# Optimization experiments

Measured on AMD Instinct MI355X. Metric: run time of the kernel, lower is better.

The kernel has to match this reference:

```python
import jax, jax.numpy as jnp
import numpy as np
import math

B, N, T, D, H, NOUT = 32, 20, 100, 4, 128, 16
E = N * (N - 1)
EPS = 1e-5

def _conv1d(x, w, b):
    # x: [M, Cin, L], w: [Cout, Cin, K] -> [M, Cout, L-K+1] (VALID, stride 1)
    y = jax.lax.conv_general_dilated(x, w, (1,), 'VALID', dimension_numbers=('NCH', 'OIH', 'NCH'))
    return y + b[None, :, None]

def _bn(x, g, b, axes, caxis):
    # training-mode batch norm (biased variance), eps as in torch
    m = jnp.mean(x, axis=axes, keepdims=True)
    v = jnp.var(x, axis=axes, keepdims=True)
    sh = [1] * x.ndim
    sh[caxis] = -1
    return (x - m) / jnp.sqrt(v + EPS) * g.reshape(sh) + b.reshape(sh)

def _mlp(x, w1, b1, w2, b2, g, bb):
    h = jax.nn.elu(x @ w1.T + b1)
    h = jax.nn.elu(h @ w2.T + b2)
    return _bn(h, g, bb, (0, 1), 2)  # BN over B*E samples per feature

def _forward(rel_rec, rel_send, inputs, conv1_w, conv1_b, bn1_g, bn1_b, conv2_w, conv2_b, bn2_g, bn2_b, pred_w, pred_b, att_w, att_b, mlp1_w1, mlp1_b1, mlp1_w2, mlp1_b2, mlp1_g, mlp1_bb, mlp2_w1, mlp2_b1, mlp2_w2, mlp2_b2, mlp2_g, mlp2_bb, mlp3_w1, mlp3_b1, mlp3_w2, mlp3_b2, mlp3_g, mlp3_bb, fc_out_w, fc_out_b):
    Bv, Nv, Tv, Dv = inputs.shape
    Ev = Nv * (Nv - 1)
    # node2edge_temporal: gather sender/receiver trajectories -> [B*E, 2D, T]
    xf = inputs.reshape(Bv, Nv, Tv * Dv)
    recv = jnp.einsum('en,bnf->bef', rel_rec, xf).reshape(Bv * Ev, Tv, Dv).transpose(0, 2, 1)
    send = jnp.einsum('en,bnf->bef', rel_send, xf).reshape(Bv * Ev, Tv, Dv).transpose(0, 2, 1)
    edges = jnp.concatenate([send, recv], axis=1)
    # CNN over time
    h = jax.nn.relu(_conv1d(edges, conv1_w, conv1_b))
    h = _bn(h, bn1_g, bn1_b, (0, 2), 1)
    L = h.shape[-1] // 2
    h = h[:, :, : 2 * L].reshape(h.shape[0], h.shape[1], L, 2).max(axis=-1)  # maxpool k=2 s=2
    h = jax.nn.relu(_conv1d(h, conv2_w, conv2_b))
    h = _bn(h, bn2_g, bn2_b, (0, 2), 1)
    pred = jnp.einsum('bct,oc->bot', h, pred_w[:, :, 0]) + pred_b[None, :, None]
    att = jax.nn.softmax(jnp.einsum('bct,oc->bot', h, att_w[:, :, 0]) + att_b[None, :, None], axis=-1)
    x = (pred * att).mean(axis=-1).reshape(Bv, Ev, -1)  # attention-weighted mean pool
    x = _mlp(x, mlp1_w1, mlp1_b1, mlp1_w2, mlp1_b2, mlp1_g, mlp1_bb)
    x_skip = x
    # edge2node: scatter-mean into receivers (divide by N)
    xn = jnp.einsum('en,beh->bnh', rel_rec, x) / Nv
    xn = _mlp(xn, mlp2_w1, mlp2_b1, mlp2_w2, mlp2_b2, mlp2_g, mlp2_bb)
    # node2edge: gather back to edges
    es = jnp.einsum('en,bnh->beh', rel_send, xn)
    er = jnp.einsum('en,bnh->beh', rel_rec, xn)
    x = jnp.concatenate([es, er, x_skip], axis=2)
    x = _mlp(x, mlp3_w1, mlp3_b1, mlp3_w2, mlp3_b2, mlp3_g, mlp3_bb)
    return x @ fc_out_w.T + fc_out_b

def setup_inputs() -> dict:
    key = jax.random.key(0)
    ks = iter(jax.random.split(key, 64))
    def rn(shape, scale):
        return jax.random.normal(next(ks), shape, dtype=jnp.float32) * scale
    def xav(fo, fi):
        return rn((fo, fi), math.sqrt(2.0 / (fo + fi)))
    inputs = rn((B, N, T, D), 1.0)
    pairs = np.array([(i, j) for i in range(N) for j in range(N) if i != j])
    eye = np.eye(N, dtype=np.float32)
    d = {'inputs': inputs,
         'rel_rec': jnp.asarray(eye[pairs[:, 0]]),
         'rel_send': jnp.asarray(eye[pairs[:, 1]])}
    d['conv1_w'] = rn((H, 2 * D, 5), math.sqrt(2.0 / (5 * H)))
    d['conv1_b'] = jnp.full((H,), 0.1, jnp.float32)
    d['bn1_g'] = jnp.ones((H,), jnp.float32); d['bn1_b'] = jnp.zeros((H,), jnp.float32)
    d['conv2_w'] = rn((H, H, 5), math.sqrt(2.0 / (5 * H)))
    d['conv2_b'] = jnp.full((H,), 0.1, jnp.float32)
    d['bn2_g'] = jnp.ones((H,), jnp.float32); d['bn2_b'] = jnp.zeros((H,), jnp.float32)
    d['pred_w'] = rn((H, H, 1), math.sqrt(2.0 / H))
    d['pred_b'] = jnp.full((H,), 0.1, jnp.float32)
    d['att_w'] = rn((1, H, 1), math.sqrt(2.0))
    d['att_b'] = jnp.full((1,), 0.1, jnp.float32)
    for nm, fi in (('mlp1', H), ('mlp2', H), ('mlp3', 3 * H)):
        d[nm + '_w1'] = xav(H, fi); d[nm + '_b1'] = jnp.full((H,), 0.1, jnp.float32)
        d[nm + '_w2'] = xav(H, H); d[nm + '_b2'] = jnp.full((H,), 0.1, jnp.float32)
        d[nm + '_g'] = jnp.ones((H,), jnp.float32); d[nm + '_bb'] = jnp.zeros((H,), jnp.float32)
    d['fc_out_w'] = xav(NOUT, H)
    d['fc_out_b'] = jnp.full((NOUT,), 0.1, jnp.float32)
    return d

def reference(inputs, rel_rec, rel_send, conv1_w, conv1_b, bn1_g, bn1_b, conv2_w, conv2_b, bn2_g, bn2_b, pred_w, pred_b, att_w, att_b, mlp1_w1, mlp1_b1, mlp1_w2, mlp1_b2, mlp1_g, mlp1_bb, mlp2_w1, mlp2_b1, mlp2_w2, mlp2_b2, mlp2_g, mlp2_bb, mlp3_w1, mlp3_b1, mlp3_w2, mlp3_b2, mlp3_g, mlp3_bb, fc_out_w, fc_out_b):
    return _forward(rel_rec, rel_send, inputs, conv1_w, conv1_b, bn1_g, bn1_b, conv2_w, conv2_b, bn2_g, bn2_b, pred_w, pred_b, att_w, att_b, mlp1_w1, mlp1_b1, mlp1_w2, mlp1_b2, mlp1_g, mlp1_bb, mlp2_w1, mlp2_b1, mlp2_w2, mlp2_b2, mlp2_g, mlp2_bb, mlp3_w1, mlp3_b1, mlp3_w2, mlp3_b2, mlp3_g, mlp3_bb, fc_out_w, fc_out_b)
```

## Files before the change

kernel.cpp:

```cpp
#include <hip/hip_runtime.h>
#include <hip/hip_bf16.h>
#include <hip/hip_fp16.h>

#define BB 32
#define NN 20
#define TT 100
#define DD 4
#define HH 128
#define EE 380
#define BE 12160
#define L1 96
#define LP 48
#define L2 44
#define NOUT 16
#define EPS 1e-5f
#define NREP 64

typedef _Float16 f16x8 __attribute__((ext_vector_type(8)));
typedef _Float16 f16x4 __attribute__((ext_vector_type(4)));
typedef _Float16 f16x2 __attribute__((ext_vector_type(2)));
typedef float f32x4 __attribute__((ext_vector_type(4)));

#define S_BN1_SC 256
#define S_BN2_SC 768
#define S_M1_SC 1280
#define S_M2_SC 1792
#define S_M3_SC 2304

#define OFF_STATS 0ULL
#define OFF_SIDX 16384ULL
#define OFF_RIDX 18432ULL
#define OFF_INC 20480ULL
#define OFF_Y23 24576ULL
#define OFF_X 149446656ULL
#define OFF_BUFA 155672576ULL
#define OFF_BUFB 161898496ULL
#define OFF_XN 168124416ULL
#define OFF_T640 168452096ULL
#define OFF_REPM 168779776ULL
#define OFF_HF16 168845312ULL
#define OFF_MP 171958272ULL
#define OFF_APACK OFF_T640
#define OFF_APACK1 (OFF_T640 + 163840ULL)
#define OFF_PWT (OFF_T640 + 180224ULL)
#define OFF_REP1 OFF_BUFA
#define OFF_REP2 (OFF_BUFA + 65536ULL)
#define MP_M1W1 0
#define MP_M1W2 16384
#define MP_M2W1 32768
#define MP_M2W2 49152
#define MP_M3W2 65536
#define MP_M3W1 81920

__device__ __forceinline__ float eluf(float v) { return v > 0.f ? v : expm1f(v); }

__global__ __launch_bounds__(256) void k_prep(const float* __restrict__ rel_rec,
                                              const float* __restrict__ rel_send,
                                              const float* __restrict__ w2,
                                              const float* __restrict__ w1,
                                              const float* __restrict__ pred_w,
                                              const float* __restrict__ m1w1,
                                              const float* __restrict__ m1w2,
                                              const float* __restrict__ m2w1,
                                              const float* __restrict__ m2w2,
                                              const float* __restrict__ m3w1,
                                              const float* __restrict__ m3w2,
                                              _Float16* __restrict__ apack,
                                              _Float16* __restrict__ apack1,
                                              float* __restrict__ pwt,
                                              _Float16* __restrict__ mp,
                                              float* rep1, float* rep2, float* repm,
                                              int* sidx, int* ridx, int* inc) {
    int b = blockIdx.x;
    int tid = threadIdx.x;
    int l = tid & 63;
    if (b < 40) {
        int f = b * 4 + (tid >> 6);
        int m0 = f & 7, ks = f >> 3, s = ks & 3, k = ks >> 2;
        int m = m0 * 16 + (l & 15);
        int cbase = 32 * s + (l >> 4) * 8;
#pragma unroll
        for (int j = 0; j < 8; ++j)
            apack[(f * 64 + l) * 8 + j] = (_Float16)w2[m * 640 + (cbase + j) * 5 + k];
    } else if (b < 44) {
        int f = (b - 40) * 4 + (tid >> 6);
        int m0 = f & 7, s = f >> 3;
        int m = m0 * 16 + (l & 15);
        int cbase = 32 * s + (l >> 4) * 8;
#pragma unroll
        for (int j = 0; j < 8; ++j) {
            int c = cbase + j;
            int k = c >> 3, ci = c & 7;
            apack1[(f * 64 + l) * 8 + j] = (k < 5) ? (_Float16)w1[m * 40 + ci * 5 + k]
                                                   : (_Float16)0.f;
        }
    } else if (b == 44) {
        for (int i = tid; i < NREP * 256; i += 256) { rep1[i] = 0.f; rep2[i] = 0.f; repm[i] = 0.f; }
        for (int e = tid; e < EE; e += 256) {
            int s = 0, r = 0;
            for (int n = 0; n < NN; ++n) {
                if (rel_send[e * NN + n] > 0.5f) s = n;
                if (rel_rec[e * NN + n] > 0.5f) r = n;
            }
            sidx[e] = s; ridx[e] = r;
        }
        __syncthreads();
        if (tid < NN) {
            int k = 0;
            for (int e = 0; e < EE; ++e)
                if (ridx[e] == tid) inc[tid * (NN - 1) + (k++)] = e;
        }
    } else if (b < 53) {
        int idx = (b - 45) * 2048 + tid;
        for (int rep = 0; rep < 8; ++rep, idx += 256) {
            int o = idx >> 7, c = idx & 127;
            pwt[c * 128 + o] = pred_w[idx];
        }
    } else {
        int idx = b - 53;
        const float* W; _Float16* dst; int K;
        if (idx < 8)       { W = m1w1; dst = mp + MP_M1W1; K = 128; }
        else if (idx < 16) { W = m1w2; dst = mp + MP_M1W2; K = 128; idx -= 8; }
        else if (idx < 24) { W = m2w1; dst = mp + MP_M2W1; K = 128; idx -= 16; }
        else if (idx < 32) { W = m2w2; dst = mp + MP_M2W2; K = 128; idx -= 24; }
        else if (idx < 40) { W = m3w2; dst = mp + MP_M3W2; K = 128; idx -= 32; }
        else               { W = m3w1; dst = mp + MP_M3W1; K = 384; idx -= 40; }
        int f = idx * 4 + (tid >> 6);
        int s = f >> 3, m0 = f & 7;
        int m = m0 * 16 + (l & 15);
        int cb = 32 * s + (l >> 4) * 8;
#pragma unroll
        for (int j = 0; j < 8; ++j)
            dst[(f * 64 + l) * 8 + j] = (_Float16)W[m * K + cb + j];
    }
}

__global__ __launch_bounds__(256) void k_conv1_stats(const float* __restrict__ inputs,
                                                     const _Float16* __restrict__ apack1,
                                                     const float* __restrict__ conv1_b,
                                                     const int* __restrict__ sidx,
                                                     const int* __restrict__ ridx,
                                                     float* rep1,
                                                     _Float16* __restrict__ y2p) {
    __shared__ __align__(16) _Float16 s_edgesT[104 * 8];
    __shared__ __align__(16) _Float16 s_y2t[48 * 136];
    int be = blockIdx.x;
    int b = be / EE, e = be - b * EE;
    int sn = sidx[e], rn = ridx[e];
    float* rep = rep1 + (be & (NREP - 1)) * 256;
    for (int i = threadIdx.x; i < 200; i += 256) {
        int side = (i >= 100) ? 1 : 0;
        int t = i - side * 100;
        int n = side ? rn : sn;
        float4 v = *(const float4*)(inputs + ((long long)(b * NN + n) * TT + t) * DD);
        f16x4 o = {(_Float16)v.x, (_Float16)v.y, (_Float16)v.z, (_Float16)v.w};
        *(f16x4*)(&s_edgesT[t * 8 + side * 4]) = o;
    }
    if (threadIdx.x < 32) s_edgesT[800 + threadIdx.x] = (_Float16)0.f;
    __syncthreads();
    int w = threadIdx.x >> 6, lane = threadIdx.x & 63;
    int quad = lane >> 4, l15 = lane & 15;
    f32x4 acc1[2][6];
#pragma unroll
    for (int m = 0; m < 2; ++m)
#pragma unroll
        for (int nt = 0; nt < 6; ++nt) acc1[m][nt] = (f32x4){0.f, 0.f, 0.f, 0.f};
    {
        const f16x8* Ap = (const f16x8*)apack1;
#pragma unroll
        for (int s = 0; s < 2; ++s) {
            f16x8 a0 = Ap[(s * 8 + 2 * w) * 64 + lane];
            f16x8 a1 = Ap[(s * 8 + 2 * w + 1) * 64 + lane];
#pragma unroll
            for (int nt = 0; nt < 6; ++nt) {
                f16x8 bfr = *(const f16x8*)(&s_edgesT[(nt * 16 + l15 + 4 * s + quad) * 8]);
                acc1[0][nt] = __builtin_amdgcn_mfma_f32_16x16x32_f16(a0, bfr, acc1[0][nt], 0, 0, 0);
                acc1[1][nt] = __builtin_amdgcn_mfma_f32_16x16x32_f16(a1, bfr, acc1[1][nt], 0, 0, 0);
            }
        }
    }
#pragma unroll
    for (int m = 0; m < 2; ++m) {
        int co0 = (2 * w + m) * 16 + quad * 4;
        float ss[4] = {0.f, 0.f, 0.f, 0.f}, qq[4] = {0.f, 0.f, 0.f, 0.f};
#pragma unroll
        for (int nt = 0; nt < 6; ++nt) {
            int t = nt * 16 + l15;
#pragma unroll
            for (int r = 0; r < 4; ++r) {
                float v = fmaxf(acc1[m][nt][r] + conv1_b[co0 + r], 0.f);
                ss[r] += v; qq[r] += v * v;
                float p = __shfl_xor(v, 1);
                if ((l15 & 1) == 0)
                    s_y2t[(t >> 1) * 136 + co0 + r] = (_Float16)fmaxf(v, p);
            }
        }
#pragma unroll
        for (int r = 0; r < 4; ++r) {
            float s = ss[r], q = qq[r];
            s += __shfl_xor(s, 1); s += __shfl_xor(s, 2); s += __shfl_xor(s, 4); s += __shfl_xor(s, 8);
            q += __shfl_xor(q, 1); q += __shfl_xor(q, 2); q += __shfl_xor(q, 4); q += __shfl_xor(q, 8);
            if (l15 == 0) {
                atomicAdd(&rep[co0 + r], s);
                atomicAdd(&rep[128 + co0 + r], q);
            }
        }
    }
    __syncthreads();
    _Float16* dst = y2p + (long long)be * 6144;
    for (int chunk = threadIdx.x; chunk < 768; chunk += 256) {
        int row = chunk >> 4, off = (chunk & 15) * 8;
        *(f16x8*)(dst + row * 128 + off) = *(const f16x8*)(&s_y2t[row * 136 + off]);
    }
}

__global__ void k_finalize_rep(float* __restrict__ rep, float* stats, int scIdx,
                               const float* __restrict__ g, const float* __restrict__ bb,
                               float inv_count) {
    int j = threadIdx.x;
    float s = 0.f, q = 0.f;
    for (int i = 0; i < NREP; ++i) {
        s += rep[i * 256 + j];
        q += rep[i * 256 + 128 + j];
    }
    for (int i = 0; i < NREP; ++i) {
        rep[i * 256 + j] = 0.f;
        rep[i * 256 + 128 + j] = 0.f;
    }
    float m = s * inv_count;
    float v = fmaxf(q * inv_count - m * m, 0.f);
    float sc = g[j] * rsqrtf(v + EPS);
    stats[scIdx + j] = sc;
    stats[scIdx + 128 + j] = bb[j] - m * sc;
}

__global__ __launch_bounds__(256) void k_conv2(_Float16* __restrict__ y23,
                                               const _Float16* __restrict__ apack,
                                               const float* __restrict__ conv2_b,
                                               const float* __restrict__ stats,
                                               float* rep2) {
    __shared__ __align__(16) _Float16 s_y2t[2][52 * 136];
    int tid = threadIdx.x;
    int be0 = blockIdx.x * 2;
    for (int i = tid; i < 544; i += 256) {
        int ed = i / 272, rem = i - ed * 272;
        ((int*)(&s_y2t[ed][48 * 136]))[rem] = 0;
    }
    {
        int c0 = (tid & 15) * 8;
        float4 sca = *(const float4*)(stats + S_BN1_SC + c0);
        float4 scb = *(const float4*)(stats + S_BN1_SC + c0 + 4);
        float4 sha = *(const float4*)(stats + S_BN1_SC + 128 + c0);
        float4 shb = *(const float4*)(stats + S_BN1_SC + 128 + c0 + 4);
        for (int i = tid; i < 1536; i += 256) {
            int ed = i / 768, rem = i - ed * 768;
            int row = rem >> 4;
            f16x8 g = *(const f16x8*)(y23 + (long long)(be0 + ed) * 6144 + row * 128 + c0);
            f16x8 o;
            o[0] = (_Float16)fmaf((float)g[0], sca.x, sha.x);
            o[1] = (_Float16)fmaf((float)g[1], sca.y, sha.y);
            o[2] = (_Float16)fmaf((float)g[2], sca.z, sha.z);
            o[3] = (_Float16)fmaf((float)g[3], sca.w, sha.w);
            o[4] = (_Float16)fmaf((float)g[4], scb.x, shb.x);
            o[5] = (_Float16)fmaf((float)g[5], scb.y, shb.y);
            o[6] = (_Float16)fmaf((float)g[6], scb.z, shb.z);
            o[7] = (_Float16)fmaf((float)g[7], scb.w, shb.w);
            *(f16x8*)(&s_y2t[ed][row * 136 + c0]) = o;
        }
    }
    __syncthreads();
    int w = tid >> 6, lane = tid & 63;
    int quad = lane >> 4, l15 = lane & 15;
    int g = w & 1, e = w >> 1;
    f32x4 acc[4][3];
#pragma unroll
    for (int m = 0; m < 4; ++m)
#pragma unroll
        for (int nt = 0; nt < 3; ++nt) acc[m][nt] = (f32x4){0.f, 0.f, 0.f, 0.f};
    const f16x8* Ap = (const f16x8*)apack;
    const char* base = (const char*)&s_y2t[e][0];
#pragma unroll
    for (int k = 0; k < 5; ++k) {
#pragma unroll
        for (int s = 0; s < 4; ++s) {
            f16x8 am[4];
#pragma unroll
            for (int m = 0; m < 4; ++m)
                am[m] = Ap[((k * 4 + s) * 8 + g * 4 + m) * 64 + lane];
#pragma unroll
            for (int nt = 0; nt < 3; ++nt) {
                f16x8 bfr = *(const f16x8*)(base + (nt * 16 + l15 + k) * 272 + 64 * s + quad * 16);
#pragma unroll
                for (int m = 0; m < 4; ++m)
                    acc[m][nt] = __builtin_amdgcn_mfma_f32_16x16x32_f16(am[m], bfr, acc[m][nt], 0, 0, 0);
            }
        }
    }
    int be = be0 + e;
    _Float16* y3 = y23 + (long long)be * 6144;
    float* rep = rep2 + (be & (NREP - 1)) * 256;
#pragma unroll
    for (int m = 0; m < 4; ++m) {
        int co0 = (g * 4 + m) * 16 + quad * 4;
        float ssum[4] = {0.f, 0.f, 0.f, 0.f}, qsum[4] = {0.f, 0.f, 0.f, 0.f};
#pragma unroll
        for (int nt = 0; nt < 3; ++nt) {
            int t = nt * 16 + l15;
            bool valid = t < 44;
#pragma unroll
            for (int r = 0; r < 4; ++r) {
                float v = fmaxf(acc[m][nt][r] + conv2_b[co0 + r], 0.f);
                if (valid) {
                    y3[(co0 + r) * 44 + t] = (_Float16)v;
                    ssum[r] += v; qsum[r] += v * v;
                }
            }
        }
#pragma unroll
        for (int r = 0; r < 4; ++r) {
            float s = ssum[r], q = qsum[r];
            s += __shfl_xor(s, 1); s += __shfl_xor(s, 2); s += __shfl_xor(s, 4); s += __shfl_xor(s, 8);
            q += __shfl_xor(q, 1); q += __shfl_xor(q, 2); q += __shfl_xor(q, 4); q += __shfl_xor(q, 8);
            if (l15 == 0) {
                atomicAdd(&rep[co0 + r], s);
                atomicAdd(&rep[128 + co0 + r], q);
            }
        }
    }
}

__global__ __launch_bounds__(256) void k_predatt(const _Float16* __restrict__ y23,
                                                 const float* __restrict__ stats,
                                                 const float* __restrict__ att_w,
                                                 const float* __restrict__ att_b,
                                                 const float* __restrict__ pwt,
                                                 const float* __restrict__ pred_b,
                                                 float* __restrict__ x) {
    __shared__ float h[128 * 45];
    __shared__ float s_att[48];
    __shared__ float s_p1[256];
    __shared__ float s_p2[256];
    __shared__ float s_sc[128], s_sh[128];
    int be = blockIdx.x, tid = threadIdx.x;
    if (tid < 128) {
        s_sc[tid] = stats[S_BN2_SC + tid];
        s_sh[tid] = stats[S_BN2_SC + 128 + tid];
    }
    __syncthreads();
    const f16x2* yp = (const f16x2*)(y23 + (long long)be * 6144);
    for (int i = tid; i < 2816; i += 256) {
        int c = i / 22, t2 = i - c * 22;
        f16x2 v = yp[i];
        float sc = s_sc[c], sh = s_sh[c];
        h[c * 45 + 2 * t2] = fmaf((float)v[0], sc, sh);
        h[c * 45 + 2 * t2 + 1] = fmaf((float)v[1], sc, sh);
    }
    __syncthreads();
    int w = tid >> 6, lane = tid & 63;
    {
        float aw0 = att_w[lane], aw1 = att_w[64 + lane];
        for (int tt = 0; tt < 11; ++tt) {
            int t = w * 11 + tt;
            float p = h[lane * 45 + t] * aw0 + h[(64 + lane) * 45 + t] * aw1;
            p += __shfl_xor(p, 1); p += __shfl_xor(p, 2); p += __shfl_xor(p, 4);
            p += __shfl_xor(p, 8); p += __shfl_xor(p, 16); p += __shfl_xor(p, 32);
            if (lane == 0) s_att[t] = p + att_b[0];
        }
    }
    __syncthreads();
    if (w == 0) {
        float v = (lane < 44) ? s_att[lane] : -1e30f;
        float m = v;
        m = fmaxf(m, __shfl_xor(m, 1)); m = fmaxf(m, __shfl_xor(m, 2));
        m = fmaxf(m, __shfl_xor(m, 4)); m = fmaxf(m, __shfl_xor(m, 8));
        m = fmaxf(m, __shfl_xor(m, 16)); m = fmaxf(m, __shfl_xor(m, 32));
        float ev = (lane < 44) ? expf(v - m) : 0.f;
        float ss = ev;
        ss += __shfl_xor(ss, 1); ss += __shfl_xor(ss, 2); ss += __shfl_xor(ss, 4);
        ss += __shfl_xor(ss, 8); ss += __shfl_xor(ss, 16); ss += __shfl_xor(ss, 32);
        if (lane < 44) s_att[lane] = ev / ss;
    }
    __syncthreads();
    {
        int c = tid & 127, hh = tid >> 7;
        float a = 0.f;
        for (int t = hh * 22; t < hh * 22 + 22; ++t) a = fmaf(h[c * 45 + t], s_att[t], a);
        s_p1[tid] = a;
    }
    __syncthreads();
    {
        int o = tid & 127, hh = tid >> 7;
        float a = 0.f;
        for (int c = hh * 64; c < hh * 64 + 64; ++c) {
            float hw = s_p1[c] + s_p1[128 + c];
            a = fmaf(pwt[c * 128 + o], hw, a);
        }
        s_p2[tid] = a;
    }
    __syncthreads();
    if (tid < 128) {
        float a = s_p2[tid] + s_p2[128 + tid] + pred_b[tid];
        x[(long long)be * 128 + tid] = a * (1.0f / 44.0f);
    }
}

template <bool IN16, bool OUT16, bool STATS>
__global__ __launch_bounds__(256) void k_linmm(const void* __restrict__ inV,
                                               const _Float16* __restrict__ wp,
                                               const float* __restrict__ bias,
                                               void* __restrict__ outV,
                                               float* __restrict__ repm) {
    __shared__ __align__(16) _Float16 s_b[64 * 136];
    int tid = threadIdx.x;
    long long r0 = (long long)blockIdx.x * 64;
    if (IN16) {
        const f16x8* src = (const f16x8*)((const _Float16*)inV + r0 * 128);
        for (int i = tid; i < 1024; i += 256) {
            int row = i >> 4, c0 = (i & 15) * 8;
            *(f16x8*)(&s_b[row * 136 + c0]) = src[i];
        }
    } else {
        const float4* src = (const float4*)((const float*)inV + r0 * 128);
        for (int i = tid; i < 2048; i += 256) {
            int row = i >> 5, c0 = (i & 31) * 4;
            float4 v = src[i];
            f16x4 o = {(_Float16)v.x, (_Float16)v.y, (_Float16)v.z, (_Float16)v.w};
            *(f16x4*)(&s_b[row * 136 + c0]) = o;
        }
    }
    __syncthreads();
    int w = tid >> 6, lane = tid & 63, quad = lane >> 4, l15 = lane & 15;
    f32x4 acc[2][4];
#pragma unroll
    for (int m = 0; m < 2; ++m)
#pragma unroll
        for (int nt = 0; nt < 4; ++nt) acc[m][nt] = (f32x4){0.f, 0.f, 0.f, 0.f};
    const f16x8* Ap = (const f16x8*)wp;
#pragma unroll
    for (int s = 0; s < 4; ++s) {
        f16x8 a0 = Ap[(s * 8 + 2 * w) * 64 + lane];
        f16x8 a1 = Ap[(s * 8 + 2 * w + 1) * 64 + lane];
#pragma unroll
        for (int nt = 0; nt < 4; ++nt) {
            f16x8 bfr = *(const f16x8*)((const char*)s_b + (nt * 16 + l15) * 272 + 64 * s + quad * 16);
            acc[0][nt] = __builtin_amdgcn_mfma_f32_16x16x32_f16(a0, bfr, acc[0][nt], 0, 0, 0);
            acc[1][nt] = __builtin_amdgcn_mfma_f32_16x16x32_f16(a1, bfr, acc[1][nt], 0, 0, 0);
        }
    }
#pragma unroll
    for (int m = 0; m < 2; ++m) {
        int j0 = (2 * w + m) * 16 + quad * 4;
        float4 bs = *(const float4*)(bias + j0);
        float ss[4] = {0.f, 0.f, 0.f, 0.f}, qq[4] = {0.f, 0.f, 0.f, 0.f};
#pragma unroll
        for (int nt = 0; nt < 4; ++nt) {
            int row = nt * 16 + l15;
            float v0 = eluf(acc[m][nt][0] + bs.x);
            float v1 = eluf(acc[m][nt][1] + bs.y);
            float v2 = eluf(acc[m][nt][2] + bs.z);
            float v3 = eluf(acc[m][nt][3] + bs.w);
            if (OUT16) {
                f16x4 o = {(_Float16)v0, (_Float16)v1, (_Float16)v2, (_Float16)v3};
                *(f16x4*)((_Float16*)outV + (r0 + row) * 128 + j0) = o;
            } else {
                float4 o = {v0, v1, v2, v3};
                *(float4*)((float*)outV + (r0 + row) * 128 + j0) = o;
            }
            if (STATS) {
                ss[0] += v0; qq[0] += v0 * v0;
                ss[1] += v1; qq[1] += v1 * v1;
                ss[2] += v2; qq[2] += v2 * v2;
                ss[3] += v3; qq[3] += v3 * v3;
            }
        }
        if (STATS) {
            float* rep = repm + (blockIdx.x & (NREP - 1)) * 256;
#pragma unroll
            for (int r = 0; r < 4; ++r) {
                float s = ss[r], q = qq[r];
                s += __shfl_xor(s, 1); s += __shfl_xor(s, 2); s += __shfl_xor(s, 4); s += __shfl_xor(s, 8);
                q += __shfl_xor(q, 1); q += __shfl_xor(q, 2); q += __shfl_xor(q, 4); q += __shfl_xor(q, 8);
                if (l15 == 0) {
                    atomicAdd(&rep[j0 + r], s);
                    atomicAdd(&rep[128 + j0 + r], q);
                }
            }
        }
    }
}

__global__ __launch_bounds__(256) void k_linmm3(const float* __restrict__ xn,
                                                const float* __restrict__ bufB,
                                                const int* __restrict__ sidx,
                                                const int* __restrict__ ridx,
                                                const float* __restrict__ stats,
                                                const _Float16* __restrict__ wp,
                                                const float* __restrict__ bias,
                                                _Float16* __restrict__ out) {
    __shared__ __align__(16) _Float16 s_b[64 * 392];
    __shared__ float s_st[4][128];
    __shared__ int s_s[64], s_r[64];
    int tid = threadIdx.x;
    long long r0 = (long long)blockIdx.x * 64;
    if (tid < 128) {
        s_st[0][tid] = stats[S_M2_SC + tid];
        s_st[1][tid] = stats[S_M2_SC + 128 + tid];
        s_st[2][tid] = stats[S_M1_SC + tid];
        s_st[3][tid] = stats[S_M1_SC + 128 + tid];
    }
    if (tid < 64) {
        int r = (int)r0 + tid, b = r / EE, ed = r - b * EE;
        s_s[tid] = (b * NN + sidx[ed]) * 128;
        s_r[tid] = (b * NN + ridx[ed]) * 128;
    }
    __syncthreads();
    for (int i = tid; i < 8192; i += 256) {
        int row = i >> 7, j = i & 127;
        float sc2 = s_st[0][j], sh2 = s_st[1][j];
        s_b[row * 392 + j] = (_Float16)fmaf(xn[s_s[row] + j], sc2, sh2);
        s_b[row * 392 + 128 + j] = (_Float16)fmaf(xn[s_r[row] + j], sc2, sh2);
        s_b[row * 392 + 256 + j] = (_Float16)fmaf(bufB[(r0 + row) * 128 + j], s_st[2][j], s_st[3][j]);
    }
    __syncthreads();
    int w = tid >> 6, lane = tid & 63, quad = lane >> 4, l15 = lane & 15;
    f32x4 acc[2][4];
#pragma unroll
    for (int m = 0; m < 2; ++m)
#pragma unroll
        for (int nt = 0; nt < 4; ++nt) acc[m][nt] = (f32x4){0.f, 0.f, 0.f, 0.f};
    const f16x8* Ap = (const f16x8*)wp;
#pragma unroll
    for (int s = 0; s < 12; ++s) {
        f16x8 a0 = Ap[(s * 8 + 2 * w) * 64 + lane];
        f16x8 a1 = Ap[(s * 8 + 2 * w + 1) * 64 + lane];
#pragma unroll
        for (int nt = 0; nt < 4; ++nt) {
            f16x8 bfr = *(const f16x8*)((const char*)s_b + (nt * 16 + l15) * 784 + 64 * s + quad * 16);
            acc[0][nt] = __builtin_amdgcn_mfma_f32_16x16x32_f16(a0, bfr, acc[0][nt], 0, 0, 0);
            acc[1][nt] = __builtin_amdgcn_mfma_f32_16x16x32_f16(a1, bfr, acc[1][nt], 0, 0, 0);
        }
    }
#pragma unroll
    for (int m = 0; m < 2; ++m) {
        int j0 = (2 * w + m) * 16 + quad * 4;
        float4 bs = *(const float4*)(bias + j0);
#pragma unroll
        for (int nt = 0; nt < 4; ++nt) {
            int row = nt * 16 + l15;
            f16x4 o = {(_Float16)eluf(acc[m][nt][0] + bs.x),
                       (_Float16)eluf(acc[m][nt][1] + bs.y),
                       (_Float16)eluf(acc[m][nt][2] + bs.z),
                       (_Float16)eluf(acc[m][nt][3] + bs.w)};
            *(f16x4*)(out + (r0 + row) * 128 + j0) = o;
        }
    }
}

__global__ __launch_bounds__(128) void k_e2n(const float* __restrict__ bufB,
                                             const int* __restrict__ inc,
                                             const float* __restrict__ stats,
                                             float* __restrict__ xn) {
    int bn = blockIdx.x;
    int b = bn / NN, n = bn - b * NN;
    int j = threadIdx.x;
    float sc = stats[S_M1_SC + j], sh = stats[S_M1_SC + 128 + j];
    float s = 0.f;
    for (int k = 0; k < NN - 1; ++k) {
        int e = inc[n * (NN - 1) + k];
        s += bufB[(long long)(b * EE + e) * 128 + j];
    }
    xn[bn * 128 + j] = (s * sc + (float)(NN - 1) * sh) * (1.0f / (float)NN);
}

__global__ __launch_bounds__(256) void k_fcout(const float* __restrict__ h2,
                                               const float* __restrict__ stats,
                                               const float* __restrict__ fcw,
                                               const float* __restrict__ fcb,
                                               float* __restrict__ out) {
    __shared__ float s_x[16 * 129];
    __shared__ float s_w[16 * 129];
    int r0 = blockIdx.x * 16;
    int tid = threadIdx.x;
    for (int i = tid; i < 16 * 128; i += 256) {
        int rr = i >> 7, j = i & 127;
        s_x[rr * 129 + j] = fmaf(h2[(long long)(r0 + rr) * 128 + j],
                                 stats[S_M3_SC + j], stats[S_M3_SC + 128 + j]);
    }
    for (int i = tid; i < 16 * 128; i += 256) {
        int o = i >> 7, j = i & 127;
        s_w[o * 129 + j] = fcw[i];
    }
    __syncthreads();
    int rl = tid >> 4, o = tid & 15;
    float a = fcb[o];
    for (int j = 0; j < 128; ++j) a = fmaf(s_x[rl * 129 + j], s_w[o * 129 + j], a);
    out[(long long)(r0 + rl) * 16 + o] = a;
}

extern "C" void kernel_launch(void* const* d_in, const int* in_sizes, int n_in,
                              void* d_out, int out_size, void* d_ws, size_t ws_size,
                              hipStream_t stream) {
    const float* inputs = (const float*)d_in[0];
    const float* rel_rec = (const float*)d_in[1];
    const float* rel_send = (const float*)d_in[2];
    const float* conv1_w = (const float*)d_in[3];
    const float* conv1_b = (const float*)d_in[4];
    const float* bn1_g = (const float*)d_in[5];
    const float* bn1_b = (const float*)d_in[6];
    const float* conv2_w = (const float*)d_in[7];
    const float* conv2_b = (const float*)d_in[8];
    const float* bn2_g = (const float*)d_in[9];
    const float* bn2_b = (const float*)d_in[10];
    const float* pred_w = (const float*)d_in[11];
    const float* pred_b = (const float*)d_in[12];
    const float* att_w = (const float*)d_in[13];
    const float* att_b = (const float*)d_in[14];
    const float* m1w1 = (const float*)d_in[15];
    const float* m1b1 = (const float*)d_in[16];
    const float* m1w2 = (const float*)d_in[17];
    const float* m1b2 = (const float*)d_in[18];
    const float* m1g = (const float*)d_in[19];
    const float* m1bb = (const float*)d_in[20];
    const float* m2w1 = (const float*)d_in[21];
    const float* m2b1 = (const float*)d_in[22];
    const float* m2w2 = (const float*)d_in[23];
    const float* m2b2 = (const float*)d_in[24];
    const float* m2g = (const float*)d_in[25];
    const float* m2bb = (const float*)d_in[26];
    const float* m3w1 = (const float*)d_in[27];
    const float* m3b1 = (const float*)d_in[28];
    const float* m3w2 = (const float*)d_in[29];
    const float* m3b2 = (const float*)d_in[30];
    const float* m3g = (const float*)d_in[31];
    const float* m3bb = (const float*)d_in[32];
    const float* fcw = (const float*)d_in[33];
    const float* fcb = (const float*)d_in[34];

    char* ws = (char*)d_ws;
    float* stats = (float*)(ws + OFF_STATS);
    int* sidx = (int*)(ws + OFF_SIDX);
    int* ridx = (int*)(ws + OFF_RIDX);
    int* inc = (int*)(ws + OFF_INC);
    _Float16* y23 = (_Float16*)(ws + OFF_Y23);
    float* x = (float*)(ws + OFF_X);
    float* bufB = (float*)(ws + OFF_BUFB);
    float* xn = (float*)(ws + OFF_XN);
    _Float16* apack = (_Float16*)(ws + OFF_APACK);
    _Float16* apack1 = (_Float16*)(ws + OFF_APACK1);
    float* pwt = (float*)(ws + OFF_PWT);
    float* rep1 = (float*)(ws + OFF_REP1);
    float* rep2 = (float*)(ws + OFF_REP2);
    float* repm = (float*)(ws + OFF_REPM);
    _Float16* hf16 = (_Float16*)(ws + OFF_HF16);
    _Float16* mp = (_Float16*)(ws + OFF_MP);
    float* outp = (float*)d_out;

    hipLaunchKernelGGL(k_prep, dim3(117), dim3(256), 0, stream,
                       rel_rec, rel_send, conv2_w, conv1_w, pred_w,
                       m1w1, m1w2, m2w1, m2w2, m3w1, m3w2,
                       apack, apack1, pwt, mp, rep1, rep2, repm, sidx, ridx, inc);
    hipLaunchKernelGGL(k_conv1_stats, dim3(BE), dim3(256), 0, stream,
                       inputs, apack1, conv1_b, sidx, ridx, rep1, y23);
    hipLaunchKernelGGL(k_finalize_rep, dim3(1), dim3(128), 0, stream,
                       rep1, stats, S_BN1_SC, bn1_g, bn1_b, 1.0f / (float)(BE * L1));
    hipLaunchKernelGGL(k_conv2, dim3(BE / 2), dim3(256), 0, stream,
                       y23, apack, conv2_b, stats, rep2);
    hipLaunchKernelGGL(k_finalize_rep, dim3(1), dim3(128), 0, stream,
                       rep2, stats, S_BN2_SC, bn2_g, bn2_b, 1.0f / (float)(BE * L2));
    hipLaunchKernelGGL(k_predatt, dim3(BE), dim3(256), 0, stream,
                       y23, stats, att_w, att_b, pwt, pred_b, x);
    hipLaunchKernelGGL((k_linmm<false, true, false>), dim3(BE / 64), dim3(256), 0, stream,
                       (const void*)x, mp + MP_M1W1, m1b1, (void*)hf16, repm);
    hipLaunchKernelGGL((k_linmm<true, false, true>), dim3(BE / 64), dim3(256), 0, stream,
                       (const void*)hf16, mp + MP_M1W2, m1b2, (void*)bufB, repm);
    hipLaunchKernelGGL(k_finalize_rep, dim3(1), dim3(128), 0, stream,
                       repm, stats, S_M1_SC, m1g, m1bb, 1.0f / (float)BE);
    hipLaunchKernelGGL(k_e2n, dim3(BB * NN), dim3(128), 0, stream, bufB, inc, stats, xn);
    hipLaunchKernelGGL((k_linmm<false, true, false>), dim3(BB * NN / 64), dim3(256), 0, stream,
                       (const void*)xn, mp + MP_M2W1, m2b1, (void*)hf16, repm);
    hipLaunchKernelGGL((k_linmm<true, false, true>), dim3(BB * NN / 64), dim3(256), 0, stream,
                       (const void*)hf16, mp + MP_M2W2, m2b2, (void*)xn, repm);
    hipLaunchKernelGGL(k_finalize_rep, dim3(1), dim3(128), 0, stream,
                       repm, stats, S_M2_SC, m2g, m2bb, 1.0f / (float)(BB * NN));
    hipLaunchKernelGGL(k_linmm3, dim3(BE / 64), dim3(256), 0, stream,
                       xn, bufB, sidx, ridx, stats, mp + MP_M3W1, m3b1, hf16);
    hipLaunchKernelGGL((k_linmm<true, false, true>), dim3(BE / 64), dim3(256), 0, stream,
                       (const void*)hf16, mp + MP_M3W2, m3b2, (void*)bufB, repm);
    hipLaunchKernelGGL(k_finalize_rep, dim3(1), dim3(128), 0, stream,
                       repm, stats, S_M3_SC, m3g, m3bb, 1.0f / (float)BE);
    hipLaunchKernelGGL(k_fcout, dim3(BE / 16), dim3(256), 0, stream, bufB, stats, fcw, fcb, outp);
    (void)in_sizes; (void)n_in; (void)out_size; (void)ws_size;
}
```

Before: 597.1 us.

## Fold BN1 affine into conv2 weights and bias, store conv2 output time-major

BN1's per-channel scale is folded into the packed conv2 weights by a new small scaling kernel, and the shift is folded into an effective conv2 bias computed in the BN1 finalize kernel. This removes the per-element normalize pass from k_conv2's shared-memory staging, which becomes a plain copy. The conv2 output is now written time-major with vector f16x4 stores, and k_predatt reads it with f16x8 loads into a transposed shared tile. The cost is an extra launch plus an in-place modification of apack, which assumes apack is repacked on every call, and some f16 rounding differences because the scale is now applied to the weights.

```diff
diff --git a/kernel.cpp b/kernel.cpp
--- a/kernel.cpp
+++ b/kernel.cpp
@@ -21,6 +21,7 @@
 typedef _Float16 f16x2 __attribute__((ext_vector_type(2)));
 typedef float f32x4 __attribute__((ext_vector_type(4)));
 
+#define S_BIAS2 0
 #define S_BN1_SC 256
 #define S_BN2_SC 768
 #define S_M1_SC 1280
@@ -234,9 +235,51 @@
     stats[scIdx + 128 + j] = bb[j] - m * sc;
 }
 
+__global__ void k_finalize_bn1(float* __restrict__ rep, float* stats,
+                               const float* __restrict__ g, const float* __restrict__ bb,
+                               const float* __restrict__ w2, const float* __restrict__ conv2_b,
+                               float inv_count) {
+    __shared__ float s_sh[128];
+    int j = threadIdx.x;
+    float s = 0.f, q = 0.f;
+    for (int i = 0; i < NREP; ++i) {
+        s += rep[i * 256 + j];
+        q += rep[i * 256 + 128 + j];
+    }
+    for (int i = 0; i < NREP; ++i) {
+        rep[i * 256 + j] = 0.f;
+        rep[i * 256 + 128 + j] = 0.f;
+    }
+    float m = s * inv_count;
+    float v = fmaxf(q * inv_count - m * m, 0.f);
+    float sc = g[j] * rsqrtf(v + EPS);
+    float sh = bb[j] - m * sc;
+    stats[S_BN1_SC + j] = sc;
+    stats[S_BN1_SC + 128 + j] = sh;
+    s_sh[j] = sh;
+    __syncthreads();
+    float acc = conv2_b[j];
+    for (int ci = 0; ci < 128; ++ci) {
+        const float* wr = w2 + j * 640 + ci * 5;
+        acc += (wr[0] + wr[1] + wr[2] + wr[3] + wr[4]) * s_sh[ci];
+    }
+    stats[S_BIAS2 + j] = acc;
+}
+
+__global__ __launch_bounds__(256) void k_scale(_Float16* __restrict__ apack,
+                                               const float* __restrict__ stats) {
+    int tid = threadIdx.x, l = tid & 63;
+    int f = blockIdx.x * 4 + (tid >> 6);
+    int s = (f >> 3) & 3;
+    int cbase = 32 * s + (l >> 4) * 8;
+    _Float16* p = apack + (f * 64 + l) * 8;
+#pragma unroll
+    for (int j = 0; j < 8; ++j)
+        p[j] = (_Float16)((float)p[j] * stats[S_BN1_SC + cbase + j]);
+}
+
 __global__ __launch_bounds__(256) void k_conv2(_Float16* __restrict__ y23,
                                                const _Float16* __restrict__ apack,
-                                               const float* __restrict__ conv2_b,
                                                const float* __restrict__ stats,
                                                float* rep2) {
     __shared__ __align__(16) _Float16 s_y2t[2][52 * 136];
@@ -246,27 +289,11 @@
         int ed = i / 272, rem = i - ed * 272;
         ((int*)(&s_y2t[ed][48 * 136]))[rem] = 0;
     }
-    {
-        int c0 = (tid & 15) * 8;
-        float4 sca = *(const float4*)(stats + S_BN1_SC + c0);
-        float4 scb = *(const float4*)(stats + S_BN1_SC + c0 + 4);
-        float4 sha = *(const float4*)(stats + S_BN1_SC + 128 + c0);
-        float4 shb = *(const float4*)(stats + S_BN1_SC + 128 + c0 + 4);
-        for (int i = tid; i < 1536; i += 256) {
-            int ed = i / 768, rem = i - ed * 768;
-            int row = rem >> 4;
-            f16x8 g = *(const f16x8*)(y23 + (long long)(be0 + ed) * 6144 + row * 128 + c0);
-            f16x8 o;
-            o[0] = (_Float16)fmaf((float)g[0], sca.x, sha.x);
-            o[1] = (_Float16)fmaf((float)g[1], sca.y, sha.y);
-            o[2] = (_Float16)fmaf((float)g[2], sca.z, sha.z);
-            o[3] = (_Float16)fmaf((float)g[3], sca.w, sha.w);
-            o[4] = (_Float16)fmaf((float)g[4], scb.x, shb.x);
-            o[5] = (_Float16)fmaf((float)g[5], scb.y, shb.y);
-            o[6] = (_Float16)fmaf((float)g[6], scb.z, shb.z);
-            o[7] = (_Float16)fmaf((float)g[7], scb.w, shb.w);
-            *(f16x8*)(&s_y2t[ed][row * 136 + c0]) = o;
-        }
+    for (int i = tid; i < 1536; i += 256) {
+        int ed = i / 768, rem = i - ed * 768;
+        int row = rem >> 4, c0 = (rem & 15) * 8;
+        *(f16x8*)(&s_y2t[ed][row * 136 + c0]) =
+            *(const f16x8*)(y23 + (long long)(be0 + ed) * 6144 + rem * 8);
     }
     __syncthreads();
     int w = tid >> 6, lane = tid & 63;
@@ -302,18 +329,22 @@
 #pragma unroll
     for (int m = 0; m < 4; ++m) {
         int co0 = (g * 4 + m) * 16 + quad * 4;
+        float4 bs = *(const float4*)(stats + S_BIAS2 + co0);
         float ssum[4] = {0.f, 0.f, 0.f, 0.f}, qsum[4] = {0.f, 0.f, 0.f, 0.f};
 #pragma unroll
         for (int nt = 0; nt < 3; ++nt) {
             int t = nt * 16 + l15;
-            bool valid = t < 44;
-#pragma unroll
-            for (int r = 0; r < 4; ++r) {
-                float v = fmaxf(acc[m][nt][r] + conv2_b[co0 + r], 0.f);
-                if (valid) {
-                    y3[(co0 + r) * 44 + t] = (_Float16)v;
-                    ssum[r] += v; qsum[r] += v * v;
-                }
+            if (t < 44) {
+                float v0 = fmaxf(acc[m][nt][0] + bs.x, 0.f);
+                float v1 = fmaxf(acc[m][nt][1] + bs.y, 0.f);
+                float v2 = fmaxf(acc[m][nt][2] + bs.z, 0.f);
+                float v3 = fmaxf(acc[m][nt][3] + bs.w, 0.f);
+                f16x4 o = {(_Float16)v0, (_Float16)v1, (_Float16)v2, (_Float16)v3};
+                *(f16x4*)(y3 + t * 128 + co0) = o;
+                ssum[0] += v0; qsum[0] += v0 * v0;
+                ssum[1] += v1; qsum[1] += v1 * v1;
+                ssum[2] += v2; qsum[2] += v2 * v2;
+                ssum[3] += v3; qsum[3] += v3 * v3;
             }
         }
 #pragma unroll
@@ -336,7 +367,7 @@
                                                  const float* __restrict__ pwt,
                                                  const float* __restrict__ pred_b,
                                                  float* __restrict__ x) {
-    __shared__ float h[128 * 45];
+    __shared__ float h[44 * 132];
     __shared__ float s_att[48];
     __shared__ float s_p1[256];
     __shared__ float s_p2[256];
@@ -347,13 +378,21 @@
         s_sh[tid] = stats[S_BN2_SC + 128 + tid];
     }
     __syncthreads();
-    const f16x2* yp = (const f16x2*)(y23 + (long long)be * 6144);
-    for (int i = tid; i < 2816; i += 256) {
-        int c = i / 22, t2 = i - c * 22;
-        f16x2 v = yp[i];
-        float sc = s_sc[c], sh = s_sh[c];
-        h[c * 45 + 2 * t2] = fmaf((float)v[0], sc, sh);
-        h[c * 45 + 2 * t2 + 1] = fmaf((float)v[1], sc, sh);
+    const _Float16* yp = y23 + (long long)be * 6144;
+    for (int i = tid; i < 704; i += 256) {
+        int t = i >> 4, c0 = (i & 15) * 8;
+        f16x8 v = *(const f16x8*)(yp + i * 8);
+        float4 a, bq;
+        a.x = fmaf((float)v[0], s_sc[c0 + 0], s_sh[c0 + 0]);
+        a.y = fmaf((float)v[1], s_sc[c0 + 1], s_sh[c0 + 1]);
+        a.z = fmaf((float)v[2], s_sc[c0 + 2], s_sh[c0 + 2]);
+        a.w = fmaf((float)v[3], s_sc[c0 + 3], s_sh[c0 + 3]);
+        bq.x = fmaf((float)v[4], s_sc[c0 + 4], s_sh[c0 + 4]);
+        bq.y = fmaf((float)v[5], s_sc[c0 + 5], s_sh[c0 + 5]);
+        bq.z = fmaf((float)v[6], s_sc[c0 + 6], s_sh[c0 + 6]);
+        bq.w = fmaf((float)v[7], s_sc[c0 + 7], s_sh[c0 + 7]);
+        *(float4*)(&h[t * 132 + c0]) = a;
+        *(float4*)(&h[t * 132 + c0 + 4]) = bq;
     }
     __syncthreads();
     int w = tid >> 6, lane = tid & 63;
@@ -361,7 +400,7 @@
         float aw0 = att_w[lane], aw1 = att_w[64 + lane];
         for (int tt = 0; tt < 11; ++tt) {
             int t = w * 11 + tt;
-            float p = h[lane * 45 + t] * aw0 + h[(64 + lane) * 45 + t] * aw1;
+            float p = h[t * 132 + lane] * aw0 + h[t * 132 + 64 + lane] * aw1;
             p += __shfl_xor(p, 1); p += __shfl_xor(p, 2); p += __shfl_xor(p, 4);
             p += __shfl_xor(p, 8); p += __shfl_xor(p, 16); p += __shfl_xor(p, 32);
             if (lane == 0) s_att[t] = p + att_b[0];
@@ -384,7 +423,7 @@
     {
         int c = tid & 127, hh = tid >> 7;
         float a = 0.f;
-        for (int t = hh * 22; t < hh * 22 + 22; ++t) a = fmaf(h[c * 45 + t], s_att[t], a);
+        for (int t = hh * 22; t < hh * 22 + 22; ++t) a = fmaf(h[t * 132 + c], s_att[t], a);
         s_p1[tid] = a;
     }
     __syncthreads();
@@ -661,10 +700,11 @@
                        apack, apack1, pwt, mp, rep1, rep2, repm, sidx, ridx, inc);
     hipLaunchKernelGGL(k_conv1_stats, dim3(BE), dim3(256), 0, stream,
                        inputs, apack1, conv1_b, sidx, ridx, rep1, y23);
-    hipLaunchKernelGGL(k_finalize_rep, dim3(1), dim3(128), 0, stream,
-                       rep1, stats, S_BN1_SC, bn1_g, bn1_b, 1.0f / (float)(BE * L1));
+    hipLaunchKernelGGL(k_finalize_bn1, dim3(1), dim3(128), 0, stream,
+                       rep1, stats, bn1_g, bn1_b, conv2_w, conv2_b, 1.0f / (float)(BE * L1));
+    hipLaunchKernelGGL(k_scale, dim3(40), dim3(256), 0, stream, apack, stats);
     hipLaunchKernelGGL(k_conv2, dim3(BE / 2), dim3(256), 0, stream,
-                       y23, apack, conv2_b, stats, rep2);
+                       y23, apack, stats, rep2);
     hipLaunchKernelGGL(k_finalize_rep, dim3(1), dim3(128), 0, stream,
                        rep2, stats, S_BN2_SC, bn2_g, bn2_b, 1.0f / (float)(BE * L2));
     hipLaunchKernelGGL(k_predatt, dim3(BE), dim3(256), 0, stream,
```

Result: slower. 613.0 us (+2.7%).
